# Kernel optimization log

Hardware: AMD Instinct MI355X
Metric: run time of the kernel (lower is better)

The kernel has to match this reference:

```python
import jax, jax.numpy as jnp
import numpy as np

B, T, D = 2, 2048, 1024
H = 16
DH = D // H
SCALE = DH ** -0.5


def setup_inputs() -> dict:
    key = jax.random.key(0)
    ks = jax.random.split(key, 10)
    s = lambda fan_in: 1.0 / np.sqrt(fan_in)
    # weights stored (in, out) so y = x @ W + b (torch Linear transposed)
    return {
        "x": jax.random.normal(ks[0], (B, T, D), dtype=jnp.float32),
        "Wqkv0": jax.random.uniform(ks[1], (D, 3 * D), jnp.float32, -s(D), s(D)),
        "bqkv0": jax.random.uniform(ks[2], (3 * D,), jnp.float32, -s(D), s(D)),
        "Wqkv1": jax.random.uniform(ks[3], (D, 3 * D), jnp.float32, -s(D), s(D)),
        "bqkv1": jax.random.uniform(ks[4], (3 * D,), jnp.float32, -s(D), s(D)),
        "Wg": jax.random.uniform(ks[5], (2 * D, D), jnp.float32, -s(2 * D), s(2 * D)),
        "bg": jax.random.uniform(ks[6], (D,), jnp.float32, -s(2 * D), s(2 * D)),
        "Wo": jax.random.uniform(ks[7], (D, D), jnp.float32, -s(D), s(D)),
        "bo": jax.random.uniform(ks[8], (D,), jnp.float32, -s(D), s(D)),
    }


def _attend(x, Wqkv, bqkv):
    # x: [B,T,D] -> qkv: [B,T,3,H,DH]
    qkv = (x @ Wqkv + bqkv).reshape(B, T, 3, H, DH)
    q, k, v = qkv[:, :, 0], qkv[:, :, 1], qkv[:, :, 2]  # [B,T,H,DH]
    scores = jnp.einsum("bqhd,bkhd->bhqk", q, k) * SCALE
    causal = jnp.tril(jnp.ones((T, T), dtype=bool))
    scores = jnp.where(causal, scores, jnp.finfo(scores.dtype).min)
    attn = jax.nn.softmax(scores, axis=-1)  # dropout is identity in eval mode
    out = jnp.einsum("bhqk,bkhd->bqhd", attn, v)
    return out.reshape(B, T, D)


def reference(x, Wqkv0, bqkv0, Wqkv1, bqkv1, Wg, bg, Wo, bo):
    pred = _attend(x, Wqkv0, bqkv0)
    output = pred
    cumulative = pred
    # n_rounds = 2 -> one correction round
    residual = x - cumulative
    correction = _attend(residual, Wqkv1, bqkv1)
    gate = jax.nn.sigmoid(jnp.concatenate([cumulative, correction], axis=-1) @ Wg + bg)
    gated = gate * correction
    output = output + gated
    return output @ Wo + bo
```

## Files before the change

### kernel.cpp

```cpp
#include <hip/hip_runtime.h>
#include <hip/hip_bf16.h>


typedef __bf16 bf16x8 __attribute__((ext_vector_type(8)));
typedef float f32x4 __attribute__((ext_vector_type(4)));

__device__ __forceinline__ unsigned short f2bf(float f) {
  union { __hip_bfloat16 h; unsigned short u; } cv;
  cv.h = __float2bfloat16(f);
  return cv.u;
}

#define GLD16(gp, lp) __builtin_amdgcn_global_load_lds(                      \
    (const __attribute__((address_space(1))) void*)(gp),                     \
    (__attribute__((address_space(3))) void*)(lp), 16, 0, 0)

__global__ __launch_bounds__(256) void prep_batch(
    const float* __restrict__ W0, __hip_bfloat16* __restrict__ Wt0,
    const float* __restrict__ W1, __hip_bfloat16* __restrict__ Wt1,
    const float* __restrict__ Wg, __hip_bfloat16* __restrict__ Wgt,
    const float* __restrict__ Wo, __hip_bfloat16* __restrict__ Wot,
    const float* __restrict__ x, __hip_bfloat16* __restrict__ xb) {
  const int bid = blockIdx.x;
  if (bid >= 9216) {
    size_t e = (((size_t)(bid - 9216)) * 256 + threadIdx.x) * 4;
    float4 v = *(const float4*)(x + e);
    ushort4 o;
    o.x = f2bf(v.x); o.y = f2bf(v.y); o.z = f2bf(v.z); o.w = f2bf(v.w);
    *(ushort4*)((unsigned short*)xb + e) = o;
    return;
  }
  const float* in; __hip_bfloat16* out; int R, C, base;
  if (bid < 3072)      { in = W0; out = Wt0; R = 1024; C = 3072; base = 0; }
  else if (bid < 6144) { in = W1; out = Wt1; R = 1024; C = 3072; base = 3072; }
  else if (bid < 8192) { in = Wg; out = Wgt; R = 2048; C = 1024; base = 6144; }
  else                 { in = Wo; out = Wot; R = 1024; C = 1024; base = 8192; }
  const int local = bid - base, nbx = C / 32;
  const int bx = (local % nbx) * 32, by = (local / nbx) * 32;
  const int tx = threadIdx.x & 31, ty = threadIdx.x >> 5;
  __shared__ float t[32][33];
#pragma unroll
  for (int i = 0; i < 32; i += 8)
    t[ty + i][tx] = in[(size_t)(by + ty + i) * C + bx + tx];
  __syncthreads();
#pragma unroll
  for (int i = 0; i < 32; i += 8)
    out[(size_t)(bx + ty + i) * R + by + tx] = __float2bfloat16(t[tx][ty + i]);
}

template <int EPI>
__global__ __launch_bounds__(256) void gemm_bf16(
    const __hip_bfloat16* __restrict__ A, const __hip_bfloat16* __restrict__ Bt,
    const float* __restrict__ bias, void* __restrict__ outp,
    const __hip_bfloat16* __restrict__ aux0, const __hip_bfloat16* __restrict__ aux1,
    int M, int N, int K) {
  __shared__ __hip_bfloat16 As[2][128 * 32];
  __shared__ __hip_bfloat16 Bs[2][128 * 32];
  const int tid = threadIdx.x;
  const int lane = tid & 63, wid = tid >> 6;
  const int wr = wid >> 1, wc = wid & 1;
  const int lr = lane & 15, lk = (lane >> 4) * 8;
  const int nbx = N >> 7;
  const int cpx = gridDim.x >> 3;
  const int swz = (blockIdx.x & 7) * cpx + (blockIdx.x >> 3);
  const size_t bcol = (size_t)(swz % nbx) * 128;
  const size_t brow = (size_t)(swz / nbx) * 128;
  f32x4 acc[4][4] = {};
#pragma unroll
  for (int r = 0; r < 2; ++r) {
    int c = tid + r * 256;
    GLD16(A + (brow + (size_t)(c >> 2)) * K + (c & 3) * 8, As[0] + c * 8);
    GLD16(Bt + (bcol + (size_t)(c >> 2)) * K + (c & 3) * 8, Bs[0] + c * 8);
  }
  __syncthreads();
  int cur = 0;
  for (int k0 = 0; k0 < K; k0 += 32) {
    const int nxt = cur ^ 1;
    if (k0 + 32 < K) {
#pragma unroll
      for (int r = 0; r < 2; ++r) {
        int c = tid + r * 256;
        GLD16(A + (brow + (size_t)(c >> 2)) * K + k0 + 32 + (c & 3) * 8,
              As[nxt] + c * 8);
        GLD16(Bt + (bcol + (size_t)(c >> 2)) * K + k0 + 32 + (c & 3) * 8,
              Bs[nxt] + c * 8);
      }
    }
    bf16x8 a[4], b[4];
#pragma unroll
    for (int m = 0; m < 4; ++m)
      a[m] = *(const bf16x8*)(As[cur] + (wr * 64 + m * 16 + lr) * 32 + lk);
#pragma unroll
    for (int n = 0; n < 4; ++n)
      b[n] = *(const bf16x8*)(Bs[cur] + (wc * 64 + n * 16 + lr) * 32 + lk);
#pragma unroll
    for (int m = 0; m < 4; ++m)
#pragma unroll
      for (int n = 0; n < 4; ++n)
        acc[m][n] = __builtin_amdgcn_mfma_f32_16x16x32_bf16(a[m], b[n], acc[m][n], 0, 0, 0);
    __syncthreads();
    cur = nxt;
  }
  const int r0 = (lane >> 4) * 4, cn = lane & 15;
#pragma unroll
  for (int m = 0; m < 4; ++m)
#pragma unroll
    for (int n = 0; n < 4; ++n) {
      size_t col = bcol + wc * 64 + n * 16 + cn;
      float bv = bias[col];
#pragma unroll
      for (int j = 0; j < 4; ++j) {
        size_t row = brow + wr * 64 + m * 16 + r0 + j;
        float v = acc[m][n][j] + bv;
        if constexpr (EPI == 1) {
          float g = 1.0f / (1.0f + __expf(-v));
          float a0 = __bfloat162float(aux0[row * 2048 + col]);
          float a1 = __bfloat162float(aux1[row * 2048 + col]);
          ((__hip_bfloat16*)outp)[row * N + col] = __float2bfloat16(g * a0 + a1);
        } else if constexpr (EPI == 2) {
          ((float*)outp)[row * N + col] = v;
        } else {
          ((__hip_bfloat16*)outp)[row * N + col] = __float2bfloat16(v);
        }
      }
    }
}

__global__ __launch_bounds__(256) void attn_kernel(
    const __hip_bfloat16* __restrict__ qkv,
    __hip_bfloat16* __restrict__ outb, int ob_off,
    const __hip_bfloat16* __restrict__ xg, __hip_bfloat16* __restrict__ residb) {
  const int b = blockIdx.z, h = blockIdx.y, qtp = blockIdx.x;
  const int qlo = qtp, qhi = 31 - qtp;
  const int q0lo = qlo * 64, q0hi = qhi * 64;
  __shared__ __hip_bfloat16 ks[2][64 * 64];
  __shared__ __hip_bfloat16 vts[2][64 * 64];
  __shared__ __hip_bfloat16 qps[8192];
  const int tid = threadIdx.x, lane = tid & 63, w = tid >> 6;
  const int lr = lane & 15, lg = lane >> 4;
  const int sw = lr & 7;
  const size_t rs = 3072;
  const __hip_bfloat16* qbh = qkv + ((size_t)b * 2048 + q0hi) * rs + h * 64;
  const __hip_bfloat16* qbl = qkv + ((size_t)b * 2048 + q0lo) * rs + h * 64;
  const __hip_bfloat16* kb = qkv + (size_t)b * 2048 * rs + 1024 + h * 64;
  const __hip_bfloat16* vb = qkv + (size_t)b * 2048 * rs + 2048 + h * 64;

  const int vrow2 = tid >> 3, vseg = tid & 7;
  float4 vr0, vr1;
#pragma unroll
  for (int r = 0; r < 2; ++r) {
    int c = tid + r * 256, row = c >> 3, p = c & 7;
    GLD16(qbh + (size_t)row * rs + (p ^ (row & 7)) * 8, qps + c * 8);
    GLD16(qbl + (size_t)row * rs + (p ^ (row & 7)) * 8, qps + 4096 + c * 8);
    GLD16(kb + (size_t)row * rs + (p ^ (row & 7)) * 8, ks[0] + c * 8);
  }
  vr0 = *(const float4*)(vb + (size_t)(2 * vrow2) * rs + vseg * 8);
  vr1 = *(const float4*)(vb + (size_t)(2 * vrow2 + 1) * rs + vseg * 8);
  __syncthreads();
  const int qrow = w * 16 + lr;
  const bf16x8 qh0 = *(const bf16x8*)(qps + qrow * 64 + ((lg) ^ (qrow & 7)) * 8);
  const bf16x8 qh1 = *(const bf16x8*)(qps + qrow * 64 + ((4 + lg) ^ (qrow & 7)) * 8);
  const bf16x8 ql0 = *(const bf16x8*)(qps + 4096 + qrow * 64 + ((lg) ^ (qrow & 7)) * 8);
  const bf16x8 ql1 = *(const bf16x8*)(qps + 4096 + qrow * 64 + ((4 + lg) ^ (qrow & 7)) * 8);
  {
    const unsigned short* u0 = (const unsigned short*)&vr0;
    const unsigned short* u1 = (const unsigned short*)&vr1;
#pragma unroll
    for (int i = 0; i < 8; ++i) {
      const int dh = vseg * 8 + i;
      const int phys = (vrow2 >> 2) ^ (dh & 7) ^ ((dh >> 3) & 7);
      unsigned int pk = (unsigned int)u0[i] | ((unsigned int)u1[i] << 16);
      *(unsigned int*)(vts[0] + dh * 64 + phys * 8 + 2 * (vrow2 & 3)) = pk;
    }
  }
  __syncthreads();

  __hip_bfloat16* psh = qps + w * 1024;
  __hip_bfloat16* psl = qps + 4096 + w * 1024;
  float m_hi = -1e30f, l_hi = 0.f, m_lo = -1e30f, l_lo = 0.f;
  f32x4 o_hi[4] = {}, o_lo[4] = {};
  int cur = 0;

  auto process = [&](const bf16x8& qa0, const bf16x8& qa1, bool diag,
                     float& m_run, float& l_run, f32x4* o, __hip_bfloat16* psw) {
    f32x4 s4[4] = {};
    __builtin_amdgcn_s_setprio(1);
#pragma unroll
    for (int n = 0; n < 4; ++n) {
      const int kr = n * 16 + lr;
      bf16x8 k0f = *(const bf16x8*)(ks[cur] + kr * 64 + ((lg) ^ sw) * 8);
      bf16x8 k1f = *(const bf16x8*)(ks[cur] + kr * 64 + ((4 + lg) ^ sw) * 8);
      s4[n] = __builtin_amdgcn_mfma_f32_16x16x32_bf16(k0f, qa0, s4[n], 0, 0, 0);
      s4[n] = __builtin_amdgcn_mfma_f32_16x16x32_bf16(k1f, qa1, s4[n], 0, 0, 0);
    }
    __builtin_amdgcn_s_setprio(0);
    float p[4][4];
    float mloc = -1e30f;
#pragma unroll
    for (int n = 0; n < 4; ++n)
#pragma unroll
      for (int j = 0; j < 4; ++j) {
        float v = s4[n][j] * 0.125f;
        if (diag && (n * 16 + lg * 4 + j) > (w * 16 + lr)) v = -1e30f;
        p[n][j] = v;
        mloc = fmaxf(mloc, v);
      }
    mloc = fmaxf(mloc, __shfl_xor(mloc, 16));
    mloc = fmaxf(mloc, __shfl_xor(mloc, 32));
    if (!__all(mloc - m_run <= 8.0f)) {
      const float mn = fmaxf(m_run, mloc);
      const float sc = __expf(m_run - mn);
      m_run = mn;
      l_run *= sc;
      float scb[4];
#pragma unroll
      for (int j = 0; j < 4; ++j) scb[j] = __shfl(sc, lg * 4 + j);
#pragma unroll
      for (int n = 0; n < 4; ++n)
#pragma unroll
        for (int j = 0; j < 4; ++j) o[n][j] *= scb[j];
    }
    float ls = 0.f;
#pragma unroll
    for (int n = 0; n < 4; ++n)
#pragma unroll
      for (int j = 0; j < 4; ++j) { p[n][j] = __expf(p[n][j] - m_run); ls += p[n][j]; }
    ls += __shfl_xor(ls, 16);
    ls += __shfl_xor(ls, 32);
    l_run += ls;
#pragma unroll
    for (int n = 0; n < 4; ++n)
#pragma unroll
      for (int j = 0; j < 4; ++j)
        psw[lr * 64 + ((n * 2 + (lg >> 1)) ^ sw) * 8 + (lg & 1) * 4 + j] =
            __float2bfloat16(p[n][j]);
    bf16x8 pa0 = *(const bf16x8*)(&psw[lr * 64 + ((lg) ^ sw) * 8]);
    bf16x8 pa1 = *(const bf16x8*)(&psw[lr * 64 + ((4 + lg) ^ sw) * 8]);
    __builtin_amdgcn_s_setprio(1);
#pragma unroll
    for (int n = 0; n < 4; ++n) {
      const int vdh = n * 16 + lr;
      const int swv = (vdh & 7) ^ ((vdh >> 3) & 7);
      bf16x8 v0f = *(const bf16x8*)(vts[cur] + vdh * 64 + ((lg) ^ swv) * 8);
      bf16x8 v1f = *(const bf16x8*)(vts[cur] + vdh * 64 + ((4 + lg) ^ swv) * 8);
      o[n] = __builtin_amdgcn_mfma_f32_16x16x32_bf16(pa0, v0f, o[n], 0, 0, 0);
      o[n] = __builtin_amdgcn_mfma_f32_16x16x32_bf16(pa1, v1f, o[n], 0, 0, 0);
    }
    __builtin_amdgcn_s_setprio(0);
  };

  for (int kvt = 0; kvt <= qhi; ++kvt) {
    const int nxt = cur ^ 1;
    const bool pf = (kvt < qhi);
    if (pf) {
      const int kv1 = (kvt + 1) * 64;
#pragma unroll
      for (int r = 0; r < 2; ++r) {
        int c = tid + r * 256, row = c >> 3, p = c & 7;
        GLD16(kb + (size_t)(kv1 + row) * rs + (p ^ (row & 7)) * 8, ks[nxt] + c * 8);
      }
      vr0 = *(const float4*)(vb + (size_t)(kv1 + 2 * vrow2) * rs + vseg * 8);
      vr1 = *(const float4*)(vb + (size_t)(kv1 + 2 * vrow2 + 1) * rs + vseg * 8);
    }
    process(qh0, qh1, kvt == qhi, m_hi, l_hi, o_hi, psh);
    if (kvt <= qlo) process(ql0, ql1, kvt == qlo, m_lo, l_lo, o_lo, psl);
    if (pf) {
      const unsigned short* u0 = (const unsigned short*)&vr0;
      const unsigned short* u1 = (const unsigned short*)&vr1;
#pragma unroll
      for (int i = 0; i < 8; ++i) {
        const int dh = vseg * 8 + i;
        const int phys = (vrow2 >> 2) ^ (dh & 7) ^ ((dh >> 3) & 7);
        unsigned int pk = (unsigned int)u0[i] | ((unsigned int)u1[i] << 16);
        *(unsigned int*)(vts[nxt] + dh * 64 + phys * 8 + 2 * (vrow2 & 3)) = pk;
      }
    }
    __syncthreads();
    cur = nxt;
  }
  const float linv_h = 1.0f / l_hi, linv_l = 1.0f / l_lo;
#pragma unroll
  for (int j = 0; j < 4; ++j) {
    const float lih = __shfl(linv_h, lg * 4 + j);
    const float lil = __shfl(linv_l, lg * 4 + j);
    size_t rowh = (size_t)b * 2048 + q0hi + w * 16 + lg * 4 + j;
    size_t rowl = (size_t)b * 2048 + q0lo + w * 16 + lg * 4 + j;
#pragma unroll
    for (int n = 0; n < 4; ++n) {
      float vh = o_hi[n][j] * lih, vl = o_lo[n][j] * lil;
      const int col = h * 64 + n * 16 + lr;
      outb[rowh * 2048 + ob_off + col] = __float2bfloat16(vh);
      outb[rowl * 2048 + ob_off + col] = __float2bfloat16(vl);
      if (ob_off == 0) {
        float xh = __bfloat162float(xg[rowh * 1024 + col]);
        float xl = __bfloat162float(xg[rowl * 1024 + col]);
        residb[rowh * 1024 + col] = __float2bfloat16(xh - vh);
        residb[rowl * 1024 + col] = __float2bfloat16(xl - vl);
      }
    }
  }
}

extern "C" void kernel_launch(void* const* d_in, const int* in_sizes, int n_in,
                              void* d_out, int out_size, void* d_ws, size_t ws_size,
                              hipStream_t stream) {
  const float* x     = (const float*)d_in[0];
  const float* Wqkv0 = (const float*)d_in[1];
  const float* bqkv0 = (const float*)d_in[2];
  const float* Wqkv1 = (const float*)d_in[3];
  const float* bqkv1 = (const float*)d_in[4];
  const float* Wg    = (const float*)d_in[5];
  const float* bg    = (const float*)d_in[6];
  const float* Wo    = (const float*)d_in[7];
  const float* bo    = (const float*)d_in[8];
  float* out = (float*)d_out;

  char* ws = (char*)d_ws;
  __hip_bfloat16* xb   = (__hip_bfloat16*)(ws);
  __hip_bfloat16* qkv  = (__hip_bfloat16*)(ws + 8388608);
  __hip_bfloat16* catb = (__hip_bfloat16*)(ws + 67108864);
  __hip_bfloat16* Wt0  = (__hip_bfloat16*)(ws + 83886080);
  __hip_bfloat16* Wt1  = (__hip_bfloat16*)(ws + 90177536);
  __hip_bfloat16* Wgt  = (__hip_bfloat16*)(ws + 96468992);
  __hip_bfloat16* Wot  = (__hip_bfloat16*)(ws + 100663296);

  prep_batch<<<13312, 256, 0, stream>>>(Wqkv0, Wt0, Wqkv1, Wt1, Wg, Wgt,
                                        Wo, Wot, x, xb);

  gemm_bf16<0><<<768, 256, 0, stream>>>(xb, Wt0, bqkv0, (void*)qkv,
                                        nullptr, nullptr, 4096, 3072, 1024);
  attn_kernel<<<dim3(16, 16, 2), 256, 0, stream>>>(qkv, catb, 0, xb, xb);
  gemm_bf16<0><<<768, 256, 0, stream>>>(xb, Wt1, bqkv1, (void*)qkv,
                                        nullptr, nullptr, 4096, 3072, 1024);
  attn_kernel<<<dim3(16, 16, 2), 256, 0, stream>>>(qkv, catb, 1024, nullptr, nullptr);
  gemm_bf16<1><<<256, 256, 0, stream>>>(catb, Wgt, bg, (void*)xb,
                                        catb + 1024, catb, 4096, 1024, 2048);
  gemm_bf16<2><<<256, 256, 0, stream>>>(xb, Wot, bo, (void*)out,
                                        nullptr, nullptr, 4096, 1024, 1024);
}
```

Before: 283.1 us.

## Split attention KV range across two blocks and merge partials (flash-decoding style)

Each attention block now processes only half of the causal KV range for its paired query tiles, doubling the grid from 512 to 1024 blocks and writing unnormalized-merged partial outputs plus row max and sum. A new merge kernel combines the two halves with log-sum-exp weights and also computes the residual. This is meant to raise occupancy on the many-CU GPU, where 512 blocks underfill the device. In exchange it adds extra global traffic for the partials and two more kernel launches, and the Q-low tile now reuses a K buffer slot in shared memory.

```diff
diff --git a/kernel.cpp b/kernel.cpp
--- a/kernel.cpp
+++ b/kernel.cpp
@@ -9,6 +9,11 @@
   union { __hip_bfloat16 h; unsigned short u; } cv;
   cv.h = __float2bfloat16(f);
   return cv.u;
+}
+__device__ __forceinline__ float bf2f(unsigned short u) {
+  union { unsigned int u; float f; } cv;
+  cv.u = (unsigned int)u << 16;
+  return cv.f;
 }
 
 #define GLD16(gp, lp) __builtin_amdgcn_global_load_lds(                      \
@@ -128,18 +133,23 @@
 
 __global__ __launch_bounds__(256) void attn_kernel(
     const __hip_bfloat16* __restrict__ qkv,
-    __hip_bfloat16* __restrict__ outb, int ob_off,
-    const __hip_bfloat16* __restrict__ xg, __hip_bfloat16* __restrict__ residb) {
-  const int b = blockIdx.z, h = blockIdx.y, qtp = blockIdx.x;
+    __hip_bfloat16* __restrict__ po, float* __restrict__ pm,
+    float* __restrict__ pl) {
+  const int zz = blockIdx.z;
+  const int b = zz & 1, hf = zz >> 1;
+  const int h = blockIdx.y, qtp = blockIdx.x;
   const int qlo = qtp, qhi = 31 - qtp;
-  const int q0lo = qlo * 64, q0hi = qhi * 64;
+  const int S = qhi + 1, s0 = (S + 1) >> 1;
+  const int k0t = hf ? s0 : 0;
+  const int k1t = hf ? S : s0;
   __shared__ __hip_bfloat16 ks[2][64 * 64];
   __shared__ __hip_bfloat16 vts[2][64 * 64];
-  __shared__ __hip_bfloat16 qps[8192];
+  __shared__ __hip_bfloat16 qps[4096];
   const int tid = threadIdx.x, lane = tid & 63, w = tid >> 6;
   const int lr = lane & 15, lg = lane >> 4;
   const int sw = lr & 7;
   const size_t rs = 3072;
+  const int q0lo = qlo * 64, q0hi = qhi * 64;
   const __hip_bfloat16* qbh = qkv + ((size_t)b * 2048 + q0hi) * rs + h * 64;
   const __hip_bfloat16* qbl = qkv + ((size_t)b * 2048 + q0lo) * rs + h * 64;
   const __hip_bfloat16* kb = qkv + (size_t)b * 2048 * rs + 1024 + h * 64;
@@ -147,21 +157,24 @@
 
   const int vrow2 = tid >> 3, vseg = tid & 7;
   float4 vr0, vr1;
-#pragma unroll
-  for (int r = 0; r < 2; ++r) {
-    int c = tid + r * 256, row = c >> 3, p = c & 7;
-    GLD16(qbh + (size_t)row * rs + (p ^ (row & 7)) * 8, qps + c * 8);
-    GLD16(qbl + (size_t)row * rs + (p ^ (row & 7)) * 8, qps + 4096 + c * 8);
-    GLD16(kb + (size_t)row * rs + (p ^ (row & 7)) * 8, ks[0] + c * 8);
-  }
-  vr0 = *(const float4*)(vb + (size_t)(2 * vrow2) * rs + vseg * 8);
-  vr1 = *(const float4*)(vb + (size_t)(2 * vrow2 + 1) * rs + vseg * 8);
+  {
+    const int kvr = k0t * 64;
+#pragma unroll
+    for (int r = 0; r < 2; ++r) {
+      int c = tid + r * 256, row = c >> 3, p = c & 7;
+      GLD16(qbh + (size_t)row * rs + (p ^ (row & 7)) * 8, qps + c * 8);
+      GLD16(qbl + (size_t)row * rs + (p ^ (row & 7)) * 8, ks[1] + c * 8);
+      GLD16(kb + (size_t)(kvr + row) * rs + (p ^ (row & 7)) * 8, ks[0] + c * 8);
+    }
+    vr0 = *(const float4*)(vb + (size_t)(kvr + 2 * vrow2) * rs + vseg * 8);
+    vr1 = *(const float4*)(vb + (size_t)(kvr + 2 * vrow2 + 1) * rs + vseg * 8);
+  }
   __syncthreads();
   const int qrow = w * 16 + lr;
   const bf16x8 qh0 = *(const bf16x8*)(qps + qrow * 64 + ((lg) ^ (qrow & 7)) * 8);
   const bf16x8 qh1 = *(const bf16x8*)(qps + qrow * 64 + ((4 + lg) ^ (qrow & 7)) * 8);
-  const bf16x8 ql0 = *(const bf16x8*)(qps + 4096 + qrow * 64 + ((lg) ^ (qrow & 7)) * 8);
-  const bf16x8 ql1 = *(const bf16x8*)(qps + 4096 + qrow * 64 + ((4 + lg) ^ (qrow & 7)) * 8);
+  const bf16x8 ql0 = *(const bf16x8*)(ks[1] + qrow * 64 + ((lg) ^ (qrow & 7)) * 8);
+  const bf16x8 ql1 = *(const bf16x8*)(ks[1] + qrow * 64 + ((4 + lg) ^ (qrow & 7)) * 8);
   {
     const unsigned short* u0 = (const unsigned short*)&vr0;
     const unsigned short* u1 = (const unsigned short*)&vr1;
@@ -175,14 +188,13 @@
   }
   __syncthreads();
 
-  __hip_bfloat16* psh = qps + w * 1024;
-  __hip_bfloat16* psl = qps + 4096 + w * 1024;
+  __hip_bfloat16* psw = qps + w * 1024;
   float m_hi = -1e30f, l_hi = 0.f, m_lo = -1e30f, l_lo = 0.f;
   f32x4 o_hi[4] = {}, o_lo[4] = {};
   int cur = 0;
 
   auto process = [&](const bf16x8& qa0, const bf16x8& qa1, bool diag,
-                     float& m_run, float& l_run, f32x4* o, __hip_bfloat16* psw) {
+                     float& m_run, float& l_run, f32x4* o) {
     f32x4 s4[4] = {};
     __builtin_amdgcn_s_setprio(1);
 #pragma unroll
@@ -249,9 +261,9 @@
     __builtin_amdgcn_s_setprio(0);
   };
 
-  for (int kvt = 0; kvt <= qhi; ++kvt) {
+  for (int kvt = k0t; kvt < k1t; ++kvt) {
     const int nxt = cur ^ 1;
-    const bool pf = (kvt < qhi);
+    const bool pf = (kvt + 1 < k1t);
     if (pf) {
       const int kv1 = (kvt + 1) * 64;
 #pragma unroll
@@ -262,8 +274,8 @@
       vr0 = *(const float4*)(vb + (size_t)(kv1 + 2 * vrow2) * rs + vseg * 8);
       vr1 = *(const float4*)(vb + (size_t)(kv1 + 2 * vrow2 + 1) * rs + vseg * 8);
     }
-    process(qh0, qh1, kvt == qhi, m_hi, l_hi, o_hi, psh);
-    if (kvt <= qlo) process(ql0, ql1, kvt == qlo, m_lo, l_lo, o_lo, psl);
+    process(qh0, qh1, kvt == qhi, m_hi, l_hi, o_hi);
+    if (kvt <= qlo) process(ql0, ql1, kvt == qlo, m_lo, l_lo, o_lo);
     if (pf) {
       const unsigned short* u0 = (const unsigned short*)&vr0;
       const unsigned short* u1 = (const unsigned short*)&vr1;
@@ -278,7 +290,9 @@
     __syncthreads();
     cur = nxt;
   }
-  const float linv_h = 1.0f / l_hi, linv_l = 1.0f / l_lo;
+  const float linv_h = (l_hi > 0.f) ? 1.0f / l_hi : 0.f;
+  const float linv_l = (l_lo > 0.f) ? 1.0f / l_lo : 0.f;
+  __hip_bfloat16* poh = po + (size_t)hf * 4096 * 1024;
 #pragma unroll
   for (int j = 0; j < 4; ++j) {
     const float lih = __shfl(linv_h, lg * 4 + j);
@@ -287,18 +301,56 @@
     size_t rowl = (size_t)b * 2048 + q0lo + w * 16 + lg * 4 + j;
 #pragma unroll
     for (int n = 0; n < 4; ++n) {
-      float vh = o_hi[n][j] * lih, vl = o_lo[n][j] * lil;
       const int col = h * 64 + n * 16 + lr;
-      outb[rowh * 2048 + ob_off + col] = __float2bfloat16(vh);
-      outb[rowl * 2048 + ob_off + col] = __float2bfloat16(vl);
-      if (ob_off == 0) {
-        float xh = __bfloat162float(xg[rowh * 1024 + col]);
-        float xl = __bfloat162float(xg[rowl * 1024 + col]);
-        residb[rowh * 1024 + col] = __float2bfloat16(xh - vh);
-        residb[rowl * 1024 + col] = __float2bfloat16(xl - vl);
-      }
-    }
-  }
+      poh[rowh * 1024 + col] = __float2bfloat16(o_hi[n][j] * lih);
+      poh[rowl * 1024 + col] = __float2bfloat16(o_lo[n][j] * lil);
+    }
+  }
+  if (lg == 0 && h == 0) {
+  }
+  if (lg == 0) {
+  }
+  if (lg == 0) {
+    const int rh = b * 2048 + q0hi + w * 16 + lr;
+    const int rl = b * 2048 + q0lo + w * 16 + lr;
+    float* pmh = pm + ((size_t)hf * 16 + h) * 4096;
+    float* plh = pl + ((size_t)hf * 16 + h) * 4096;
+    pmh[rh] = m_hi; plh[rh] = l_hi;
+    pmh[rl] = m_lo; plh[rl] = l_lo;
+  }
+}
+
+template <int DO_RESID>
+__global__ __launch_bounds__(256) void attn_merge(
+    const __hip_bfloat16* __restrict__ po, const float* __restrict__ pm,
+    const float* __restrict__ pl, __hip_bfloat16* __restrict__ outb, int ob_off,
+    const __hip_bfloat16* __restrict__ xg, __hip_bfloat16* __restrict__ residb) {
+  const int t = blockIdx.x * 256 + threadIdx.x;
+  const int row = t >> 7, c8 = (t & 127) * 8;
+  const int h = c8 >> 6;
+  const float m0 = pm[(size_t)h * 4096 + row], l0 = pl[(size_t)h * 4096 + row];
+  const float m1 = pm[(size_t)(16 + h) * 4096 + row], l1 = pl[(size_t)(16 + h) * 4096 + row];
+  const float m = fmaxf(m0, m1);
+  float w0 = l0 * __expf(m0 - m), w1 = l1 * __expf(m1 - m);
+  const float inv = 1.0f / (w0 + w1);
+  w0 *= inv; w1 *= inv;
+  const size_t base = (size_t)row * 1024 + c8;
+  uint4 a = *(const uint4*)((const unsigned short*)po + base);
+  uint4 bq = *(const uint4*)((const unsigned short*)po + (size_t)4096 * 1024 + base);
+  const unsigned short* ua = (const unsigned short*)&a;
+  const unsigned short* ub = (const unsigned short*)&bq;
+  unsigned short om[8], rm[8];
+#pragma unroll
+  for (int i = 0; i < 8; ++i) {
+    float v = bf2f(ua[i]) * w0 + bf2f(ub[i]) * w1;
+    om[i] = f2bf(v);
+    if constexpr (DO_RESID) {
+      rm[i] = f2bf(bf2f(((const unsigned short*)xg)[base + i]) - v);
+    }
+  }
+  *(uint4*)((unsigned short*)outb + (size_t)row * 2048 + ob_off + c8) = *(uint4*)om;
+  if constexpr (DO_RESID)
+    *(uint4*)((unsigned short*)residb + base) = *(uint4*)rm;
 }
 
 extern "C" void kernel_launch(void* const* d_in, const int* in_sizes, int n_in,
@@ -318,6 +370,9 @@
   char* ws = (char*)d_ws;
   __hip_bfloat16* xb   = (__hip_bfloat16*)(ws);
   __hip_bfloat16* qkv  = (__hip_bfloat16*)(ws + 8388608);
+  __hip_bfloat16* po   = (__hip_bfloat16*)(ws + 33554432);
+  float*          pm   = (float*)(ws + 50331648);
+  float*          pl   = (float*)(ws + 50855936);
   __hip_bfloat16* catb = (__hip_bfloat16*)(ws + 67108864);
   __hip_bfloat16* Wt0  = (__hip_bfloat16*)(ws + 83886080);
   __hip_bfloat16* Wt1  = (__hip_bfloat16*)(ws + 90177536);
@@ -326,13 +381,14 @@
 
   prep_batch<<<13312, 256, 0, stream>>>(Wqkv0, Wt0, Wqkv1, Wt1, Wg, Wgt,
                                         Wo, Wot, x, xb);
-
   gemm_bf16<0><<<768, 256, 0, stream>>>(xb, Wt0, bqkv0, (void*)qkv,
                                         nullptr, nullptr, 4096, 3072, 1024);
-  attn_kernel<<<dim3(16, 16, 2), 256, 0, stream>>>(qkv, catb, 0, xb, xb);
+  attn_kernel<<<dim3(16, 16, 4), 256, 0, stream>>>(qkv, po, pm, pl);
+  attn_merge<1><<<2048, 256, 0, stream>>>(po, pm, pl, catb, 0, xb, xb);
   gemm_bf16<0><<<768, 256, 0, stream>>>(xb, Wt1, bqkv1, (void*)qkv,
                                         nullptr, nullptr, 4096, 3072, 1024);
-  attn_kernel<<<dim3(16, 16, 2), 256, 0, stream>>>(qkv, catb, 1024, nullptr, nullptr);
+  attn_kernel<<<dim3(16, 16, 4), 256, 0, stream>>>(qkv, po, pm, pl);
+  attn_merge<0><<<2048, 256, 0, stream>>>(po, pm, pl, catb, 1024, nullptr, nullptr);
   gemm_bf16<1><<<256, 256, 0, stream>>>(catb, Wgt, bg, (void*)xb,
                                         catb + 1024, catb, 4096, 1024, 2048);
   gemm_bf16<2><<<256, 256, 0, stream>>>(xb, Wot, bo, (void*)out,
```

Result: slower. 293.7 us (+3.7%).
